# Kernel tuning notes

Hardware: AMD Instinct MI355X
Metric: run time of the kernel (lower is better)

Reference implementation:

```python
import jax, jax.numpy as jnp
import numpy as np

D = 1024
D_HEAD = 64
N_PC = 1024
N_JOINTS = 128
L = N_PC + N_JOINTS  # 1152, == max_seq_len so cache read == fresh k/v at start_pos=0
N_HEADS = D // D_HEAD


def _block_mask():
    # True = attend. pc tokens attend pc tokens (full); joint tokens attend all pc
    # tokens plus causal among joints; pc tokens never attend joint tokens.
    i = jnp.arange(L)[:, None]
    j = jnp.arange(L)[None, :]
    return (j < N_PC) | ((i >= N_PC) & (j >= N_PC) & (j <= i))


def setup_inputs() -> dict:
    key = jax.random.key(0)
    kx, kqkv, kfc = jax.random.split(key, 3)
    s = 1.0 / np.sqrt(D)
    x = jax.random.normal(kx, (1, L, D), dtype=jnp.float32)
    w_qkv = jax.random.normal(kqkv, (3 * D, D), dtype=jnp.float32) * s  # torch Linear weight [out,in]
    w_fc = jax.random.normal(kfc, (D, D), dtype=jnp.float32) * s
    return {"x": x, "w_qkv": w_qkv, "w_fc": w_fc}


def reference(x, w_qkv, w_fc):
    b, l, _ = x.shape
    qkv = jnp.einsum('bld,ed->ble', x, w_qkv)  # [b, l, 3d]
    q, k, v = jnp.split(qkv, 3, axis=-1)

    def heads(t):  # [b, l, d] -> [b, nh, l, dh]
        return t.reshape(b, l, N_HEADS, D_HEAD).transpose(0, 2, 1, 3)

    q, k, v = heads(q), heads(k), heads(v)
    # KV-cache write + read at start_pos=0 with seq_len==max_seq_len is identity.
    scale = 1.0 / np.sqrt(D_HEAD)
    scores = jnp.einsum('bhqd,bhkd->bhqk', q, k) * scale
    mask = _block_mask()
    scores = jnp.where(mask[None, None, :, :], scores, jnp.finfo(scores.dtype).min)
    attn = jax.nn.softmax(scores, axis=-1)
    out = jnp.einsum('bhqk,bhkd->bhqd', attn, v)  # [b, nh, l, dh]
    out = out.transpose(0, 2, 1, 3).reshape(b, l, D)
    return jnp.einsum('bld,ed->ble', out, w_fc)
```

## Files before the change

kernel.cpp:

```cpp
#include <hip/hip_runtime.h>
#include <hip/hip_bf16.h>


typedef short bf16x8 __attribute__((ext_vector_type(8)));
typedef float f32x4 __attribute__((ext_vector_type(4)));
typedef float f32x16 __attribute__((ext_vector_type(16)));

#define L_SEQ   1152
#define NPC     1024
#define DMODEL  1024
#define TD      3072
#define NHEADS  16
#define DHEAD   64
#define NT32    36

__device__ __forceinline__ void gld_lds16(const void* g, void* l) {
  __builtin_amdgcn_global_load_lds((const __attribute__((address_space(1))) void*)g,
                                   (__attribute__((address_space(3))) void*)l,
                                   16, 0, 0);
}

template <int N>
__device__ __forceinline__ void s_wait_vmcnt() {
  if constexpr (N == 0)       asm volatile("s_waitcnt vmcnt(0)" ::: "memory");
  else if constexpr (N == 2)  asm volatile("s_waitcnt vmcnt(2)" ::: "memory");
  else if constexpr (N == 4)  asm volatile("s_waitcnt vmcnt(4)" ::: "memory");
  else if constexpr (N == 6)  asm volatile("s_waitcnt vmcnt(6)" ::: "memory");
  else if constexpr (N == 8)  asm volatile("s_waitcnt vmcnt(8)" ::: "memory");
  else if constexpr (N == 12) asm volatile("s_waitcnt vmcnt(12)" ::: "memory");
  else if constexpr (N == 16) asm volatile("s_waitcnt vmcnt(16)" ::: "memory");
  else static_assert(N == 0, "add vmcnt case");
}

__global__ void cvt_all(const float* __restrict__ x, const float* __restrict__ wq,
                        const float* __restrict__ wf,
                        __hip_bfloat16* __restrict__ xb,
                        __hip_bfloat16* __restrict__ wqb,
                        __hip_bfloat16* __restrict__ wfb) {
  const int NX = 1152 * 1024 / 4, NQ = 3072 * 1024 / 4;
  int i = blockIdx.x * blockDim.x + threadIdx.x;
  const float* s; __hip_bfloat16* d; int j;
  if (i < NX) { s = x; d = xb; j = i; }
  else if (i < NX + NQ) { s = wq; d = wqb; j = i - NX; }
  else { s = wf; d = wfb; j = i - NX - NQ; }
  float4 v = ((const float4*)s)[j];
  __align__(8) __hip_bfloat16 o[4];
  o[0] = __float2bfloat16(v.x);
  o[1] = __float2bfloat16(v.y);
  o[2] = __float2bfloat16(v.z);
  o[3] = __float2bfloat16(v.w);
  *(uint2*)&d[(size_t)j * 4] = *(const uint2*)o;
}

template <int BM, int BN, int MODE, typename OT>
__global__ __launch_bounds__(256) void gemm_bt(
    const __hip_bfloat16* __restrict__ A,
    const __hip_bfloat16* __restrict__ B,
    OT* __restrict__ C,
    __hip_bfloat16* __restrict__ kT,
    __hip_bfloat16* __restrict__ vT,
    int M, int N, int K, int MT) {
  constexpr int WMT = BM / 2, WNT = BN / 2;
  constexpr int MI = WMT / 16, NI = WNT / 16;
  constexpr int ACH = BM * 8, BCH = BN * 8;
  constexpr int S = (ACH + BCH) / 256;
  __shared__ __align__(16) __hip_bfloat16 As[3][BM * 64];
  __shared__ __align__(16) __hip_bfloat16 Bs[3][BN * 64];

  const int tid = threadIdx.x, lane = tid & 63, w = tid >> 6;
  const int wm = w >> 1, wn = w & 1, l15 = lane & 15, lg = lane >> 4;
  const int chunk = (int)gridDim.x >> 3;
  const int wgid = ((int)blockIdx.x & 7) * chunk + ((int)blockIdx.x >> 3);
  const int m0 = (wgid % MT) * BM, n0 = (wgid / MT) * BN;

  f32x4 acc[MI][NI] = {};

  auto stage = [&](int b, int kt) {
    const __hip_bfloat16* Ag = A + (size_t)m0 * K + kt;
    const __hip_bfloat16* Bg = B + (size_t)n0 * K + kt;
#pragma unroll
    for (int c = tid; c < ACH; c += 256) {
      int r = c >> 3, gc = (c & 7) ^ (r & 7);
      gld_lds16(Ag + (size_t)r * K + gc * 8, &As[b][c * 8]);
    }
#pragma unroll
    for (int c = tid; c < BCH; c += 256) {
      int r = c >> 3, gc = (c & 7) ^ (r & 7);
      gld_lds16(Bg + (size_t)r * K + gc * 8, &Bs[b][c * 8]);
    }
  };

  const int NK = K >> 6;
  stage(0, 0);
  stage(1, 64);
  stage(2, 128);

  int buf = 0;
  for (int t = 0; t < NK; ++t) {
    if (t < NK - 2)       s_wait_vmcnt<2 * S>();
    else if (t == NK - 2) s_wait_vmcnt<S>();
    else                  s_wait_vmcnt<0>();
    __builtin_amdgcn_s_barrier();
    __builtin_amdgcn_sched_barrier(0);

#pragma unroll
    for (int kk = 0; kk < 2; ++kk) {
      bf16x8 af[MI], bfr[NI];
#pragma unroll
      for (int i = 0; i < MI; ++i) {
        int r = wm * WMT + i * 16 + l15;
        af[i] = *(const bf16x8*)&As[buf][(r * 8 + (((kk << 2) + lg) ^ (r & 7))) * 8];
      }
#pragma unroll
      for (int i = 0; i < NI; ++i) {
        int r = wn * WNT + i * 16 + l15;
        bfr[i] = *(const bf16x8*)&Bs[buf][(r * 8 + (((kk << 2) + lg) ^ (r & 7))) * 8];
      }
#pragma unroll
      for (int mi = 0; mi < MI; ++mi)
#pragma unroll
        for (int ni = 0; ni < NI; ++ni)
          acc[mi][ni] = __builtin_amdgcn_mfma_f32_16x16x32_bf16(
              af[mi], bfr[ni], acc[mi][ni], 0, 0, 0);
    }

    __builtin_amdgcn_sched_barrier(0);
    __builtin_amdgcn_s_barrier();
    __builtin_amdgcn_sched_barrier(0);
    if (t + 3 < NK) stage(buf, (t + 3) * 64);
    buf = (buf + 1 == 3) ? 0 : buf + 1;
  }

  if constexpr (MODE == 0) {
#pragma unroll
    for (int mi = 0; mi < MI; ++mi)
#pragma unroll
      for (int ni = 0; ni < NI; ++ni) {
        int rb = m0 + wm * WMT + mi * 16 + lg * 4;
        int cb = n0 + wn * WNT + ni * 16 + l15;
#pragma unroll
        for (int r = 0; r < 4; ++r)
          C[(size_t)(rb + r) * N + cb] = acc[mi][ni][r];
      }
  } else if (n0 < 2 * DMODEL) {
    const bool isQ = (n0 < DMODEL);
    const float scl = isQ ? 0.18033688f : 1.0f;
    __hip_bfloat16* dst = isQ ? (__hip_bfloat16*)C : kT;
    const int nb = isQ ? n0 : (n0 - DMODEL);
    constexpr int TS2 = BN + 8;
    __hip_bfloat16* T = &As[0][0];
    static_assert(BM * TS2 * 2 <= 3 * BM * 64 * 2, "bounce too big");
    __syncthreads();
#pragma unroll
    for (int mi = 0; mi < MI; ++mi)
#pragma unroll
      for (int ni = 0; ni < NI; ++ni) {
        int ml = wm * WMT + mi * 16 + lg * 4;
        int nl = wn * WNT + ni * 16 + l15;
#pragma unroll
        for (int r = 0; r < 4; ++r)
          T[(ml + r) * TS2 + nl] = __float2bfloat16(acc[mi][ni][r] * scl);
      }
    __syncthreads();
#pragma unroll
    for (int c = tid; c < (BM * BN) / 8; c += 256) {
      int ml = c >> 4, dc = c & 15;
      bf16x8 v = *(const bf16x8*)&T[ml * TS2 + dc * 8];
      int dfull = nb + dc * 8;
      int hh = dfull >> 6, dh = dfull & 63;
      int g = m0 + ml;
      size_t off = ((size_t)(hh * NT32 + (g >> 5))) * 2048 +
                   (size_t)((dh >> 4) * 64 + ((dh >> 3) & 1) * 32 + (g & 31)) * 8;
      *(bf16x8*)&dst[off] = v;
    }
  } else {
    constexpr int TS = BM + 8;
    __hip_bfloat16* T = &As[0][0];
    static_assert(BN * TS * 2 <= 3 * BM * 64 * 2, "bounce too big");
    __syncthreads();
#pragma unroll
    for (int mi = 0; mi < MI; ++mi)
#pragma unroll
      for (int ni = 0; ni < NI; ++ni) {
        int e = wn * WNT + ni * 16 + l15;
        int l = wm * WMT + mi * 16 + lg * 4;
        __align__(8) __hip_bfloat16 o4[4];
#pragma unroll
        for (int r = 0; r < 4; ++r) o4[r] = __float2bfloat16(acc[mi][ni][r]);
        *(uint2*)&T[e * TS + l] = *(const uint2*)o4;
      }
    __syncthreads();
#pragma unroll
    for (int c = tid; c < (BN * BM) / 8; c += 256) {
      int dl = c >> 3, kvc = (c & 7) * 8;
      bf16x8 v = *(const bf16x8*)&T[dl * TS + kvc];
      int dfull = n0 - 2 * DMODEL + dl;
      int hh = dfull >> 6, dh = dfull & 63;
      int kvg = m0 + kvc;
      size_t off = ((size_t)(hh * NT32 + (kvg >> 5))) * 2048 +
                   (size_t)((((kvg >> 4) & 1) * 2 + (dh >> 5)) * 64 +
                            ((kvg >> 3) & 1) * 32 + (dh & 31)) * 8;
      *(bf16x8*)&vT[off] = v;
    }
  }
}

__global__ __launch_bounds__(256) void attn32(
    const __hip_bfloat16* __restrict__ qT,
    const __hip_bfloat16* __restrict__ kT,
    const __hip_bfloat16* __restrict__ vT,
    __hip_bfloat16* __restrict__ attnb) {
  const int wgid = ((int)blockIdx.x & 7) * 72 + ((int)blockIdx.x >> 3);
  const int h = wgid / NT32, qt = wgid % NT32;
  const int q0 = qt * 32;
  const int tid = threadIdx.x, lane = tid & 63, w = tid >> 6;
  const int l31 = lane & 31, hi = lane >> 5;

  __shared__ __align__(16) float Osh[4][32][68];
  __shared__ float Lsh[4][32];

  const __hip_bfloat16* qtp = qT + ((size_t)h * NT32 + qt) * 2048;
  bf16x8 qf0 = *(const bf16x8*)(qtp + (0 * 64 + lane) * 8);
  bf16x8 qf1 = *(const bf16x8*)(qtp + (1 * 64 + lane) * 8);
  bf16x8 qf2 = *(const bf16x8*)(qtp + (2 * 64 + lane) * 8);
  bf16x8 qf3 = *(const bf16x8*)(qtp + (3 * 64 + lane) * 8);

  const int q = q0 + l31;
  const int lim = (q < NPC) ? NPC : (q + 1);
  const int nst = (q0 < NPC) ? 32 : ((q0 + 32) >> 5);
  const int tbeg = (w * nst) / 4, tend = ((w + 1) * nst) / 4;

  const __hip_bfloat16* ktp = kT + (size_t)h * NT32 * 2048;
  const __hip_bfloat16* vtp = vT + (size_t)h * NT32 * 2048;

  float lsum = 0.f;
  f32x16 oA = {}, oB = {};

  bf16x8 kA[4], vA[4], kB[4], vB[4];
  auto LD = [&](bf16x8 (&kf)[4], bf16x8 (&vf)[4], int t) {
    const __hip_bfloat16* kp = ktp + (size_t)t * 2048;
    const __hip_bfloat16* vp = vtp + (size_t)t * 2048;
#pragma unroll
    for (int c = 0; c < 4; ++c) kf[c] = *(const bf16x8*)(kp + (c * 64 + lane) * 8);
#pragma unroll
    for (int c = 0; c < 4; ++c) vf[c] = *(const bf16x8*)(vp + (c * 64 + lane) * 8);
  };

  auto BODY = [&](bf16x8 (&kf)[4], bf16x8 (&vf)[4], int t) {
    f32x16 S = {};
    __builtin_amdgcn_s_setprio(1);
    S = __builtin_amdgcn_mfma_f32_32x32x16_bf16(kf[0], qf0, S, 0, 0, 0);
    S = __builtin_amdgcn_mfma_f32_32x32x16_bf16(kf[1], qf1, S, 0, 0, 0);
    S = __builtin_amdgcn_mfma_f32_32x32x16_bf16(kf[2], qf2, S, 0, 0, 0);
    S = __builtin_amdgcn_mfma_f32_32x32x16_bf16(kf[3], qf3, S, 0, 0, 0);
    __builtin_amdgcn_s_setprio(0);
    const int kv0 = t << 5;
    float p[16];
#pragma unroll
    for (int r = 0; r < 16; ++r) p[r] = exp2f(S[r]);
    if (kv0 >= NPC) {
#pragma unroll
      for (int r = 0; r < 16; ++r) {
        int kv = kv0 + (r & 3) + 8 * (r >> 2) + 4 * hi;
        if (kv >= lim) p[r] = 0.f;
      }
    }
#pragma unroll
    for (int r = 0; r < 16; ++r) lsum += p[r];
    unsigned W[8];
#pragma unroll
    for (int g = 0; g < 2; ++g) {
      unsigned x0, x1, y0, y1;
      asm("v_cvt_pk_bf16_f32 %0, %1, %2" : "=v"(x0) : "v"(p[g*8+0]), "v"(p[g*8+1]));
      asm("v_cvt_pk_bf16_f32 %0, %1, %2" : "=v"(x1) : "v"(p[g*8+4]), "v"(p[g*8+5]));
      asm("v_cvt_pk_bf16_f32 %0, %1, %2" : "=v"(y0) : "v"(p[g*8+2]), "v"(p[g*8+3]));
      asm("v_cvt_pk_bf16_f32 %0, %1, %2" : "=v"(y1) : "v"(p[g*8+6]), "v"(p[g*8+7]));
      asm("v_permlane32_swap_b32 %0, %1" : "+v"(x0), "+v"(x1));
      asm("v_permlane32_swap_b32 %0, %1" : "+v"(y0), "+v"(y1));
      W[g*4+0] = x0; W[g*4+1] = y0; W[g*4+2] = x1; W[g*4+3] = y1;
    }
    bf16x8 pa0, pa1;
    __builtin_memcpy(&pa0, &W[0], 16);
    __builtin_memcpy(&pa1, &W[4], 16);
    __builtin_amdgcn_s_setprio(1);
    oA = __builtin_amdgcn_mfma_f32_32x32x16_bf16(pa0, vf[0], oA, 0, 0, 0);
    oB = __builtin_amdgcn_mfma_f32_32x32x16_bf16(pa0, vf[1], oB, 0, 0, 0);
    oA = __builtin_amdgcn_mfma_f32_32x32x16_bf16(pa1, vf[2], oA, 0, 0, 0);
    oB = __builtin_amdgcn_mfma_f32_32x32x16_bf16(pa1, vf[3], oB, 0, 0, 0);
    __builtin_amdgcn_s_setprio(0);
  };

  LD(kA, vA, tbeg);
  int st = tbeg;
  for (; st + 2 <= tend; st += 2) {
    LD(kB, vB, st + 1);
    BODY(kA, vA, st);
    LD(kA, vA, (st + 2 < tend) ? (st + 2) : st);
    BODY(kB, vB, st + 1);
  }
  if (st < tend) BODY(kA, vA, st);

  lsum += __shfl_xor(lsum, 32);

#pragma unroll
  for (int r = 0; r < 16; ++r) {
    int qr = (r & 3) + 8 * (r >> 2) + 4 * hi;
    Osh[w][qr][l31] = oA[r];
    Osh[w][qr][32 + l31] = oB[r];
  }
  if (lane < 32) Lsh[w][l31] = lsum;
  __syncthreads();

  const int qq = tid >> 3, d8 = (tid & 7) * 8;
  float inv = 1.0f / (Lsh[0][qq] + Lsh[1][qq] + Lsh[2][qq] + Lsh[3][qq]);
  __align__(16) __hip_bfloat16 o8[8];
#pragma unroll
  for (int j = 0; j < 8; ++j) {
    float o = Osh[0][qq][d8 + j] + Osh[1][qq][d8 + j] +
              Osh[2][qq][d8 + j] + Osh[3][qq][d8 + j];
    o8[j] = __float2bfloat16(o * inv);
  }
  *(int4*)&attnb[(size_t)(q0 + qq) * DMODEL + h * DHEAD + d8] = *(const int4*)o8;
}

extern "C" void kernel_launch(void* const* d_in, const int* in_sizes, int n_in,
                              void* d_out, int out_size, void* d_ws, size_t ws_size,
                              hipStream_t stream) {
  const float* x     = (const float*)d_in[0];
  const float* w_qkv = (const float*)d_in[1];
  const float* w_fc  = (const float*)d_in[2];
  float* out = (float*)d_out;

  char* ws = (char*)d_ws;
  __hip_bfloat16* xb    = (__hip_bfloat16*)(ws + 0);
  __hip_bfloat16* wqkvb = (__hip_bfloat16*)(ws + 2359296);
  __hip_bfloat16* wfcb  = (__hip_bfloat16*)(ws + 8650752);
  __hip_bfloat16* qTb   = (__hip_bfloat16*)(ws + 10747904);
  __hip_bfloat16* kTb   = (__hip_bfloat16*)(ws + 13107200);
  __hip_bfloat16* vTb   = (__hip_bfloat16*)(ws + 15466496);
  __hip_bfloat16* attnb = (__hip_bfloat16*)(ws + 17825792);

  cvt_all<<<5248, 256, 0, stream>>>(x, w_qkv, w_fc, xb, wqkvb, wfcb);

  gemm_bt<64, 128, 1, __hip_bfloat16><<<432, 256, 0, stream>>>(
      xb, wqkvb, qTb, kTb, vTb, L_SEQ, TD, DMODEL, 18);

  attn32<<<576, 256, 0, stream>>>(qTb, kTb, vTb, attnb);

  gemm_bt<64, 64, 0, float><<<288, 256, 0, stream>>>(
      attnb, wfcb, out, nullptr, nullptr, L_SEQ, DMODEL, DMODEL, 18);
}
```

Baseline: 52.78 us.

## Split attention KV range across eight waves and prefetch two tiles ahead

The attention kernel moves from 256 to 512 threads per block. The KV-tile range for each 32-query tile is now split across eight waves instead of four, with the shared-memory partial O and row sums widened to match and the final reduction rewritten to sum eight partials. The K/V register double-buffer is restructured so the next tile's loads are issued earlier. exp2f is replaced by the hardware exp2 builtin. This aims to shorten the per-block serial loop and add memory-level parallelism, at the cost of doubled LDS use, more reduction work, and possibly lower occupancy.

```diff
diff --git a/kernel.cpp b/kernel.cpp
--- a/kernel.cpp
+++ b/kernel.cpp
@@ -56,8 +56,7 @@
 __global__ __launch_bounds__(256) void gemm_bt(
     const __hip_bfloat16* __restrict__ A,
     const __hip_bfloat16* __restrict__ B,
-    OT* __restrict__ C,
-    __hip_bfloat16* __restrict__ kT,
+    OT* __restrict__ C, __hip_bfloat16* __restrict__ kT,
     __hip_bfloat16* __restrict__ vT,
     int M, int N, int K, int MT) {
   constexpr int WMT = BM / 2, WNT = BN / 2;
@@ -149,7 +148,6 @@
     const int nb = isQ ? n0 : (n0 - DMODEL);
     constexpr int TS2 = BN + 8;
     __hip_bfloat16* T = &As[0][0];
-    static_assert(BM * TS2 * 2 <= 3 * BM * 64 * 2, "bounce too big");
     __syncthreads();
 #pragma unroll
     for (int mi = 0; mi < MI; ++mi)
@@ -176,7 +174,6 @@
   } else {
     constexpr int TS = BM + 8;
     __hip_bfloat16* T = &As[0][0];
-    static_assert(BN * TS * 2 <= 3 * BM * 64 * 2, "bounce too big");
     __syncthreads();
 #pragma unroll
     for (int mi = 0; mi < MI; ++mi)
@@ -205,7 +202,7 @@
   }
 }
 
-__global__ __launch_bounds__(256) void attn32(
+__global__ __launch_bounds__(512) void attn32(
     const __hip_bfloat16* __restrict__ qT,
     const __hip_bfloat16* __restrict__ kT,
     const __hip_bfloat16* __restrict__ vT,
@@ -216,8 +213,8 @@
   const int tid = threadIdx.x, lane = tid & 63, w = tid >> 6;
   const int l31 = lane & 31, hi = lane >> 5;
 
-  __shared__ __align__(16) float Osh[4][32][68];
-  __shared__ float Lsh[4][32];
+  __shared__ __align__(16) float Osh[8][32][68];
+  __shared__ float Lsh[8][32];
 
   const __hip_bfloat16* qtp = qT + ((size_t)h * NT32 + qt) * 2048;
   bf16x8 qf0 = *(const bf16x8*)(qtp + (0 * 64 + lane) * 8);
@@ -228,7 +225,7 @@
   const int q = q0 + l31;
   const int lim = (q < NPC) ? NPC : (q + 1);
   const int nst = (q0 < NPC) ? 32 : ((q0 + 32) >> 5);
-  const int tbeg = (w * nst) / 4, tend = ((w + 1) * nst) / 4;
+  const int tbeg = (w * nst) >> 3, tend = ((w + 1) * nst) >> 3;
 
   const __hip_bfloat16* ktp = kT + (size_t)h * NT32 * 2048;
   const __hip_bfloat16* vtp = vT + (size_t)h * NT32 * 2048;
@@ -257,7 +254,7 @@
     const int kv0 = t << 5;
     float p[16];
 #pragma unroll
-    for (int r = 0; r < 16; ++r) p[r] = exp2f(S[r]);
+    for (int r = 0; r < 16; ++r) p[r] = __builtin_amdgcn_exp2f(S[r]);
     if (kv0 >= NPC) {
 #pragma unroll
       for (int r = 0; r < 16; ++r) {
@@ -291,12 +288,13 @@
   };
 
   LD(kA, vA, tbeg);
+  if (tbeg + 1 < tend) LD(kB, vB, tbeg + 1);
   int st = tbeg;
   for (; st + 2 <= tend; st += 2) {
-    LD(kB, vB, st + 1);
     BODY(kA, vA, st);
     LD(kA, vA, (st + 2 < tend) ? (st + 2) : st);
     BODY(kB, vB, st + 1);
+    if (st + 3 < tend) LD(kB, vB, st + 3);
   }
   if (st < tend) BODY(kA, vA, st);
 
@@ -311,16 +309,20 @@
   if (lane < 32) Lsh[w][l31] = lsum;
   __syncthreads();
 
-  const int qq = tid >> 3, d8 = (tid & 7) * 8;
-  float inv = 1.0f / (Lsh[0][qq] + Lsh[1][qq] + Lsh[2][qq] + Lsh[3][qq]);
-  __align__(16) __hip_bfloat16 o8[8];
-#pragma unroll
-  for (int j = 0; j < 8; ++j) {
-    float o = Osh[0][qq][d8 + j] + Osh[1][qq][d8 + j] +
-              Osh[2][qq][d8 + j] + Osh[3][qq][d8 + j];
-    o8[j] = __float2bfloat16(o * inv);
-  }
-  *(int4*)&attnb[(size_t)(q0 + qq) * DMODEL + h * DHEAD + d8] = *(const int4*)o8;
+  const int qq = tid >> 4, d4 = (tid & 15) * 4;
+  float ls = 0.f;
+#pragma unroll
+  for (int ww = 0; ww < 8; ++ww) ls += Lsh[ww][qq];
+  float inv = 1.0f / ls;
+  __align__(8) __hip_bfloat16 o4[4];
+#pragma unroll
+  for (int j = 0; j < 4; ++j) {
+    float o = 0.f;
+#pragma unroll
+    for (int ww = 0; ww < 8; ++ww) o += Osh[ww][qq][d4 + j];
+    o4[j] = __float2bfloat16(o * inv);
+  }
+  *(uint2*)&attnb[(size_t)(q0 + qq) * DMODEL + h * DHEAD + d4] = *(const uint2*)o4;
 }
 
 extern "C" void kernel_launch(void* const* d_in, const int* in_sizes, int n_in,
@@ -345,7 +347,7 @@
   gemm_bt<64, 128, 1, __hip_bfloat16><<<432, 256, 0, stream>>>(
       xb, wqkvb, qTb, kTb, vTb, L_SEQ, TD, DMODEL, 18);
 
-  attn32<<<576, 256, 0, stream>>>(qTb, kTb, vTb, attnb);
+  attn32<<<576, 512, 0, stream>>>(qTb, kTb, vTb, attnb);
 
   gemm_bt<64, 64, 0, float><<<288, 256, 0, stream>>>(
       attnb, wfcb, out, nullptr, nullptr, L_SEQ, DMODEL, DMODEL, 18);
```

Result: no change. 53.28 us (+0.9%).

## Software-pipeline attention with two waves per block and split QK accumulators

Applied to the files above, without the earlier changes.

The attention kernel now runs two waves per block instead of four, so each wave covers half of the key/value tiles. The loop is restructured so K and V loads are issued separately and the QK MFMA for the next tile runs before the softmax and PV of the current tile. The QK product is split into two independent accumulation chains, and exp2 uses the hardware intrinsic. This aims to hide load and MFMA latency and cut the cross-wave LDS reduction, at the cost of fewer resident waves and a longer serial chain per wave.

```diff
diff --git a/kernel.cpp b/kernel.cpp
--- a/kernel.cpp
+++ b/kernel.cpp
@@ -56,8 +56,7 @@
 __global__ __launch_bounds__(256) void gemm_bt(
     const __hip_bfloat16* __restrict__ A,
     const __hip_bfloat16* __restrict__ B,
-    OT* __restrict__ C,
-    __hip_bfloat16* __restrict__ kT,
+    OT* __restrict__ C, __hip_bfloat16* __restrict__ kT,
     __hip_bfloat16* __restrict__ vT,
     int M, int N, int K, int MT) {
   constexpr int WMT = BM / 2, WNT = BN / 2;
@@ -149,7 +148,6 @@
     const int nb = isQ ? n0 : (n0 - DMODEL);
     constexpr int TS2 = BN + 8;
     __hip_bfloat16* T = &As[0][0];
-    static_assert(BM * TS2 * 2 <= 3 * BM * 64 * 2, "bounce too big");
     __syncthreads();
 #pragma unroll
     for (int mi = 0; mi < MI; ++mi)
@@ -176,7 +174,6 @@
   } else {
     constexpr int TS = BM + 8;
     __hip_bfloat16* T = &As[0][0];
-    static_assert(BN * TS * 2 <= 3 * BM * 64 * 2, "bounce too big");
     __syncthreads();
 #pragma unroll
     for (int mi = 0; mi < MI; ++mi)
@@ -205,7 +202,7 @@
   }
 }
 
-__global__ __launch_bounds__(256) void attn32(
+__global__ __launch_bounds__(128) void attn32(
     const __hip_bfloat16* __restrict__ qT,
     const __hip_bfloat16* __restrict__ kT,
     const __hip_bfloat16* __restrict__ vT,
@@ -216,8 +213,8 @@
   const int tid = threadIdx.x, lane = tid & 63, w = tid >> 6;
   const int l31 = lane & 31, hi = lane >> 5;
 
-  __shared__ __align__(16) float Osh[4][32][68];
-  __shared__ float Lsh[4][32];
+  __shared__ __align__(16) float Osh[2][32][68];
+  __shared__ float Lsh[2][32];
 
   const __hip_bfloat16* qtp = qT + ((size_t)h * NT32 + qt) * 2048;
   bf16x8 qf0 = *(const bf16x8*)(qtp + (0 * 64 + lane) * 8);
@@ -228,36 +225,43 @@
   const int q = q0 + l31;
   const int lim = (q < NPC) ? NPC : (q + 1);
   const int nst = (q0 < NPC) ? 32 : ((q0 + 32) >> 5);
-  const int tbeg = (w * nst) / 4, tend = ((w + 1) * nst) / 4;
+  const int tbeg = (w * nst) >> 1, tend = ((w + 1) * nst) >> 1;
 
   const __hip_bfloat16* ktp = kT + (size_t)h * NT32 * 2048;
   const __hip_bfloat16* vtp = vT + (size_t)h * NT32 * 2048;
 
   float lsum = 0.f;
   f32x16 oA = {}, oB = {};
-
   bf16x8 kA[4], vA[4], kB[4], vB[4];
-  auto LD = [&](bf16x8 (&kf)[4], bf16x8 (&vf)[4], int t) {
+  float p[16];
+  bf16x8 pa0, pa1;
+
+  auto LDk = [&](bf16x8 (&kf)[4], int t) {
     const __hip_bfloat16* kp = ktp + (size_t)t * 2048;
+#pragma unroll
+    for (int c = 0; c < 4; ++c) kf[c] = *(const bf16x8*)(kp + (c * 64 + lane) * 8);
+  };
+  auto LDv = [&](bf16x8 (&vf)[4], int t) {
     const __hip_bfloat16* vp = vtp + (size_t)t * 2048;
 #pragma unroll
-    for (int c = 0; c < 4; ++c) kf[c] = *(const bf16x8*)(kp + (c * 64 + lane) * 8);
-#pragma unroll
     for (int c = 0; c < 4; ++c) vf[c] = *(const bf16x8*)(vp + (c * 64 + lane) * 8);
   };
 
-  auto BODY = [&](bf16x8 (&kf)[4], bf16x8 (&vf)[4], int t) {
-    f32x16 S = {};
+  auto QK = [&](bf16x8 (&kf)[4]) -> f32x16 {
+    f32x16 S0 = {}, S1 = {};
     __builtin_amdgcn_s_setprio(1);
-    S = __builtin_amdgcn_mfma_f32_32x32x16_bf16(kf[0], qf0, S, 0, 0, 0);
-    S = __builtin_amdgcn_mfma_f32_32x32x16_bf16(kf[1], qf1, S, 0, 0, 0);
-    S = __builtin_amdgcn_mfma_f32_32x32x16_bf16(kf[2], qf2, S, 0, 0, 0);
-    S = __builtin_amdgcn_mfma_f32_32x32x16_bf16(kf[3], qf3, S, 0, 0, 0);
+    S0 = __builtin_amdgcn_mfma_f32_32x32x16_bf16(kf[0], qf0, S0, 0, 0, 0);
+    S1 = __builtin_amdgcn_mfma_f32_32x32x16_bf16(kf[2], qf2, S1, 0, 0, 0);
+    S0 = __builtin_amdgcn_mfma_f32_32x32x16_bf16(kf[1], qf1, S0, 0, 0, 0);
+    S1 = __builtin_amdgcn_mfma_f32_32x32x16_bf16(kf[3], qf3, S1, 0, 0, 0);
     __builtin_amdgcn_s_setprio(0);
+    return S0 + S1;
+  };
+
+  auto FIN = [&](const f32x16& S, int t) {
+#pragma unroll
+    for (int r = 0; r < 16; ++r) p[r] = __builtin_amdgcn_exp2f(S[r]);
     const int kv0 = t << 5;
-    float p[16];
-#pragma unroll
-    for (int r = 0; r < 16; ++r) p[r] = exp2f(S[r]);
     if (kv0 >= NPC) {
 #pragma unroll
       for (int r = 0; r < 16; ++r) {
@@ -267,6 +271,9 @@
     }
 #pragma unroll
     for (int r = 0; r < 16; ++r) lsum += p[r];
+  };
+
+  auto PACK = [&]() {
     unsigned W[8];
 #pragma unroll
     for (int g = 0; g < 2; ++g) {
@@ -279,9 +286,11 @@
       asm("v_permlane32_swap_b32 %0, %1" : "+v"(y0), "+v"(y1));
       W[g*4+0] = x0; W[g*4+1] = y0; W[g*4+2] = x1; W[g*4+3] = y1;
     }
-    bf16x8 pa0, pa1;
     __builtin_memcpy(&pa0, &W[0], 16);
     __builtin_memcpy(&pa1, &W[4], 16);
+  };
+
+  auto PV = [&](bf16x8 (&vf)[4]) {
     __builtin_amdgcn_s_setprio(1);
     oA = __builtin_amdgcn_mfma_f32_32x32x16_bf16(pa0, vf[0], oA, 0, 0, 0);
     oB = __builtin_amdgcn_mfma_f32_32x32x16_bf16(pa0, vf[1], oB, 0, 0, 0);
@@ -290,15 +299,21 @@
     __builtin_amdgcn_s_setprio(0);
   };
 
-  LD(kA, vA, tbeg);
+  LDk(kA, tbeg); LDv(vA, tbeg);
+  LDk(kB, tbeg + 1); LDv(vB, tbeg + 1);
+  f32x16 S = QK(kA);
   int st = tbeg;
   for (; st + 2 <= tend; st += 2) {
-    LD(kB, vB, st + 1);
-    BODY(kA, vA, st);
-    LD(kA, vA, (st + 2 < tend) ? (st + 2) : st);
-    BODY(kB, vB, st + 1);
-  }
-  if (st < tend) BODY(kA, vA, st);
+    f32x16 S2 = QK(kB);
+    if (st + 2 < tend) LDk(kA, st + 2);
+    FIN(S, st); PACK(); PV(vA);
+    if (st + 2 < tend) LDv(vA, st + 2);
+    if (st + 2 < tend) S = QK(kA);
+    if (st + 3 < tend) LDk(kB, st + 3);
+    FIN(S2, st + 1); PACK(); PV(vB);
+    if (st + 3 < tend) LDv(vB, st + 3);
+  }
+  if (st < tend) { FIN(S, st); PACK(); PV(vA); }
 
   lsum += __shfl_xor(lsum, 32);
 
@@ -311,16 +326,19 @@
   if (lane < 32) Lsh[w][l31] = lsum;
   __syncthreads();
 
-  const int qq = tid >> 3, d8 = (tid & 7) * 8;
-  float inv = 1.0f / (Lsh[0][qq] + Lsh[1][qq] + Lsh[2][qq] + Lsh[3][qq]);
-  __align__(16) __hip_bfloat16 o8[8];
-#pragma unroll
-  for (int j = 0; j < 8; ++j) {
-    float o = Osh[0][qq][d8 + j] + Osh[1][qq][d8 + j] +
-              Osh[2][qq][d8 + j] + Osh[3][qq][d8 + j];
-    o8[j] = __float2bfloat16(o * inv);
-  }
-  *(int4*)&attnb[(size_t)(q0 + qq) * DMODEL + h * DHEAD + d8] = *(const int4*)o8;
+  const int qq = tid >> 2, d16 = (tid & 3) * 16;
+  float inv = 1.0f / (Lsh[0][qq] + Lsh[1][qq]);
+#pragma unroll
+  for (int g = 0; g < 2; ++g) {
+    __align__(16) __hip_bfloat16 o8[8];
+#pragma unroll
+    for (int j = 0; j < 8; ++j) {
+      float o = Osh[0][qq][d16 + g * 8 + j] + Osh[1][qq][d16 + g * 8 + j];
+      o8[j] = __float2bfloat16(o * inv);
+    }
+    *(int4*)&attnb[(size_t)(q0 + qq) * DMODEL + h * DHEAD + d16 + g * 8] =
+        *(const int4*)o8;
+  }
 }
 
 extern "C" void kernel_launch(void* const* d_in, const int* in_sizes, int n_in,
@@ -345,7 +363,7 @@
   gemm_bt<64, 128, 1, __hip_bfloat16><<<432, 256, 0, stream>>>(
       xb, wqkvb, qTb, kTb, vTb, L_SEQ, TD, DMODEL, 18);
 
-  attn32<<<576, 256, 0, stream>>>(qTb, kTb, vTb, attnb);
+  attn32<<<576, 128, 0, stream>>>(qTb, kTb, vTb, attnb);
 
   gemm_bt<64, 64, 0, float><<<288, 256, 0, stream>>>(
       attnb, wfcb, out, nullptr, nullptr, L_SEQ, DMODEL, DMODEL, 18);
```

New measurement: 56.71 us. +7.5%, slower.
